# Performance work log

Hardware: AMD Instinct MI355X
Metric: run time of the kernel (lower is better)

Reference implementation:

```python
import jax, jax.numpy as jnp
import numpy as np

V = 50000   # nodes
E = 600000  # edges
D = 256     # node_feat_size == graph_feat_size
K = 20      # hardcoded Kronecker projection dim
OUT = 256   # out_dim

def layer_norm(x, g, b, eps=1e-5):
    mu = jnp.mean(x, axis=-1, keepdims=True)
    var = jnp.var(x, axis=-1, keepdims=True)
    return (x - mu) * jax.lax.rsqrt(var + eps) * g + b

def setup_inputs() -> dict:
    key = jax.random.key(0)
    ks = jax.random.split(key, 12)
    def rn(k, shape, s=0.05):
        return jax.random.normal(k, shape, dtype=jnp.float32) * s
    return dict(
        node_feats=jax.random.normal(ks[0], (V, D), dtype=jnp.float32),
        src=jax.random.randint(ks[1], (E,), 0, V),
        dst=jax.random.randint(ks[2], (E,), 0, V),
        # KroneckerMessage.proj_node: Linear(D,20)+LN(20)
        Wp=rn(ks[3], (D, K)), bp=jnp.zeros((K,), jnp.float32),
        gp=jnp.ones((K,), jnp.float32), betap=jnp.zeros((K,), jnp.float32),
        # KroneckerMessage.proj_kron: Linear(400,OUT)+LN(OUT)
        Wk=rn(ks[4], (K * K, OUT)), bk=jnp.zeros((OUT,), jnp.float32),
        gk=jnp.ones((OUT,), jnp.float32), betak=jnp.zeros((OUT,), jnp.float32),
        # project_edge: Linear(2D,1)
        We=rn(ks[5], (2 * D, 1)), be=jnp.zeros((1,), jnp.float32),
        # AttentiveGRU2.project_node: Linear(D, graph_feat_size=D)
        Wn=rn(ks[6], (D, D)), bn=jnp.zeros((D,), jnp.float32),
        # GRUCell(input=D, hidden=D), torch layout [3H, in]
        W_ih=rn(ks[7], (3 * D, D)), W_hh=rn(ks[8], (3 * D, D)),
        b_ih=jnp.zeros((3 * D,), jnp.float32), b_hh=jnp.zeros((3 * D,), jnp.float32),
        # layer_norm after GRU
        g_ln=jnp.ones((D,), jnp.float32), beta_ln=jnp.zeros((D,), jnp.float32),
        # concat_proj: Linear(D+OUT, D)+LN(D)
        Wc=rn(ks[9], (D + OUT, D)), bc=jnp.zeros((D,), jnp.float32),
        gc=jnp.ones((D,), jnp.float32), betac=jnp.zeros((D,), jnp.float32),
    )

def reference(node_feats, src, dst, Wp, bp, gp, betap, Wk, bk, gk, betak,
              We, be, Wn, bn, W_ih, W_hh, b_ih, b_hh, g_ln, beta_ln,
              Wc, bc, gc, betac):
    Vn = node_feats.shape[0]
    En = src.shape[0]
    # --- KroneckerMessage branch ---
    npj = jax.nn.relu(layer_norm(node_feats @ Wp + bp, gp, betap))        # [V, 20]
    kron = jnp.einsum('ea,ek->eak', npj[src], npj[dst]).reshape(En, -1)    # [E, 400]
    kron = jax.nn.relu(layer_norm(kron @ Wk + bk, gk, betak))              # [E, OUT]
    kron_feat = jax.ops.segment_sum(kron, dst, num_segments=Vn)           # [V, OUT]
    # --- edge attention logits (he = [dst_hv, src_hv]) ---
    he = jnp.concatenate([node_feats[dst], node_feats[src]], axis=1)       # [E, 2D]
    logits = jax.nn.relu(he @ We + be)                                     # [E, 1]
    # --- edge softmax grouped by destination node ---
    m = jax.ops.segment_max(logits, dst, num_segments=Vn)                  # [V, 1]
    ex = jnp.exp(logits - m[dst])
    denom = jax.ops.segment_sum(ex, dst, num_segments=Vn)
    a = ex / denom[dst]                                                    # [E, 1]
    # --- weighted src-feature aggregation ---
    hv = node_feats @ Wn + bn                                              # [V, D]
    context = jax.nn.relu(jax.ops.segment_sum(hv[src] * a, dst, num_segments=Vn))
    # --- GRUCell(context, node_feats), torch semantics ---
    gi = context @ W_ih.T + b_ih
    gh = node_feats @ W_hh.T + b_hh
    i_r, i_z, i_n = jnp.split(gi, 3, axis=1)
    h_r, h_z, h_n = jnp.split(gh, 3, axis=1)
    r = jax.nn.sigmoid(i_r + h_r)
    z = jax.nn.sigmoid(i_z + h_z)
    n = jnp.tanh(i_n + r * h_n)
    h = (1.0 - z) * n + z * node_feats
    gru_out = layer_norm(jax.nn.relu(h), g_ln, beta_ln)                    # [V, D]
    # --- concat + projection ---
    cat = jnp.concatenate([gru_out, kron_feat], axis=1)                    # [V, D+OUT]
    return jax.nn.relu(layer_norm(cat @ Wc + bc, gc, betac))               # [V, D]
```

## Files before the change

kernel.cpp:

```cpp
#include <hip/hip_runtime.h>
#include <hip/hip_bf16.h>
#include <math.h>

#define KG 4
#define KCHUNK 128

typedef __attribute__((ext_vector_type(8))) short bfrag;
typedef __attribute__((ext_vector_type(4))) float cfrag;

__device__ __forceinline__ ushort f2bf(float f) {
    __hip_bfloat16 h = __float2bfloat16(f);
    return *(ushort*)&h;
}
__device__ __forceinline__ float bf2f(ushort u) {
    __hip_bfloat16 h;
    *(ushort*)&h = u;
    return __bfloat162float(h);
}

__device__ __forceinline__ void blockSum2(float& s1, float& s2, float* red) {
    #pragma unroll
    for (int off = 32; off > 0; off >>= 1) {
        s1 += __shfl_xor(s1, off);
        s2 += __shfl_xor(s2, off);
    }
    int lane = threadIdx.x & 63, wid = threadIdx.x >> 6;
    if (lane == 0) { red[wid] = s1; red[4 + wid] = s2; }
    __syncthreads();
    s1 = red[0] + red[1] + red[2] + red[3];
    s2 = red[4] + red[5] + red[6] + red[7];
}

__device__ __forceinline__ float dppWaveSum(float x) {
    float t;
    t = __int_as_float(__builtin_amdgcn_update_dpp(0, __float_as_int(x), 0x111, 0xf, 0xf, true)); x += t;
    t = __int_as_float(__builtin_amdgcn_update_dpp(0, __float_as_int(x), 0x112, 0xf, 0xf, true)); x += t;
    t = __int_as_float(__builtin_amdgcn_update_dpp(0, __float_as_int(x), 0x114, 0xf, 0xf, true)); x += t;
    t = __int_as_float(__builtin_amdgcn_update_dpp(0, __float_as_int(x), 0x118, 0xf, 0xf, true)); x += t;
    t = __int_as_float(__builtin_amdgcn_update_dpp(0, __float_as_int(x), 0x142, 0xf, 0xf, true)); x += t;
    t = __int_as_float(__builtin_amdgcn_update_dpp(0, __float_as_int(x), 0x143, 0xf, 0xf, true)); x += t;
    return __int_as_float(__builtin_amdgcn_readlane(__float_as_int(x), 63));
}

__device__ __forceinline__ float sigmoidf(float x) { return 1.0f / (1.0f + expf(-x)); }

__global__ __launch_bounds__(256) void cast_bf16_kernel(
    const float* __restrict__ x, ushort* __restrict__ y, int n)
{
    int i = (blockIdx.x * 256 + threadIdx.x) * 4;
    if (i < n) {
        float4 v = *(const float4*)(x + i);
        ushort4 o;
        o.x = f2bf(v.x); o.y = f2bf(v.y); o.z = f2bf(v.z); o.w = f2bf(v.w);
        *(ushort4*)(y + i) = o;
    }
}

__global__ __launch_bounds__(256) void prep_w_kernel(
    const float* __restrict__ Wn, const float* __restrict__ Wih,
    const float* __restrict__ Whh, const float* __restrict__ Wc,
    const float* __restrict__ b_ih, const float* __restrict__ b_hh,
    const float* __restrict__ Wp, const float* __restrict__ bp,
    ushort* __restrict__ BTn, ushort* __restrict__ BTrz,
    ushort* __restrict__ BTin, ushort* __restrict__ BThn,
    ushort* __restrict__ BTc, float* __restrict__ bias_rz,
    ushort* __restrict__ BTp, float* __restrict__ bp_pad)
{
    int id = blockIdx.x * 256 + threadIdx.x;
    if (id < 262144) {
        int n = id >> 9, k = id & 511;
        float v = (k < 256) ? Wih[n * 256 + k] : Whh[n * 256 + k - 256];
        BTrz[id] = f2bf(v);
    } else if (id < 327680) {
        int j = id - 262144; int n = j >> 8, k = j & 255;
        BTin[j] = f2bf(Wih[(512 + n) * 256 + k]);
    } else if (id < 393216) {
        int j = id - 327680; int n = j >> 8, k = j & 255;
        BThn[j] = f2bf(Whh[(512 + n) * 256 + k]);
    } else if (id < 458752) {
        int j = id - 393216; int n = j >> 8, k = j & 255;
        BTn[j] = f2bf(Wn[k * 256 + n]);
    } else if (id < 589824) {
        int j = id - 458752; int n = j >> 9, k = j & 511;
        BTc[j] = f2bf(Wc[k * 256 + n]);
    } else if (id < 590336) {
        int n = id - 589824;
        bias_rz[n] = b_ih[n] + b_hh[n];
    } else if (id < 623104) {
        int j = id - 590336; int n = j >> 8, k = j & 255;
        BTp[j] = f2bf((n < 20) ? Wp[k * 20 + n] : 0.f);
    } else if (id < 623232) {
        int n = id - 623104;
        bp_pad[n] = (n < 20) ? bp[n] : 0.f;
    }
}

__global__ __launch_bounds__(256) void mfma_gemm_kernel(
    const ushort* __restrict__ A1, const ushort* __restrict__ A2, int ksplit, int lda,
    const ushort* __restrict__ B, const float* __restrict__ bias,
    void* __restrict__ Cout, int store_bf16,
    int M, int N, int K, int ldc)
{
    __shared__ ushort As[128 * 64];
    __shared__ ushort Bs[128 * 64];
    int t = threadIdx.x;
    int m0 = blockIdx.x * 128, n0 = blockIdx.y * 128;
    int w = t >> 6, lane = t & 63;
    int q = lane >> 4, r = lane & 15;
    int wm = (w & 1) * 64, wn = (w >> 1) * 64;

    cfrag acc[4][4] = {};

    int srow_base = t >> 3;
    int skc = t & 7;

    for (int k0 = 0; k0 < K; k0 += 64) {
        const ushort* Ap; int kb;
        if (k0 < ksplit) { Ap = A1; kb = k0; } else { Ap = A2; kb = k0 - ksplit; }
        int4 av[4], bv[4];
        #pragma unroll
        for (int i = 0; i < 4; ++i) {
            int row = i * 32 + srow_base;
            int grow = m0 + row;
            av[i] = make_int4(0, 0, 0, 0);
            if (grow < M) av[i] = *(const int4*)(Ap + (size_t)grow * lda + kb + skc * 8);
            bv[i] = *(const int4*)(B + (size_t)(n0 + row) * K + k0 + skc * 8);
        }
        __syncthreads();
        #pragma unroll
        for (int i = 0; i < 4; ++i) {
            int row = i * 32 + srow_base;
            int off = row * 64 + ((skc ^ (row & 7)) * 8);
            *(int4*)&As[off] = av[i];
            *(int4*)&Bs[off] = bv[i];
        }
        __syncthreads();
        #pragma unroll
        for (int s = 0; s < 2; ++s) {
            bfrag af[4], bfr[4];
            int kc = s * 4 + q;
            #pragma unroll
            for (int mi = 0; mi < 4; ++mi) {
                int arow = wm + mi * 16 + r;
                af[mi] = *(const bfrag*)&As[arow * 64 + ((kc ^ (arow & 7)) * 8)];
            }
            #pragma unroll
            for (int ni = 0; ni < 4; ++ni) {
                int brow = wn + ni * 16 + r;
                bfr[ni] = *(const bfrag*)&Bs[brow * 64 + ((kc ^ (brow & 7)) * 8)];
            }
            #pragma unroll
            for (int mi = 0; mi < 4; ++mi)
                #pragma unroll
                for (int ni = 0; ni < 4; ++ni)
                    acc[mi][ni] = __builtin_amdgcn_mfma_f32_16x16x32_bf16(
                        af[mi], bfr[ni], acc[mi][ni], 0, 0, 0);
        }
    }

    float bvld[4];
    #pragma unroll
    for (int ni = 0; ni < 4; ++ni) bvld[ni] = bias[n0 + wn + ni * 16 + r];
    #pragma unroll
    for (int mi = 0; mi < 4; ++mi) {
        #pragma unroll
        for (int v = 0; v < 4; ++v) {
            int grow = m0 + wm + mi * 16 + q * 4 + v;
            if (grow >= M) continue;
            #pragma unroll
            for (int ni = 0; ni < 4; ++ni) {
                int gcol = n0 + wn + ni * 16 + r;
                if (gcol >= N) continue;
                float val = acc[mi][ni][v] + bvld[ni];
                if (store_bf16) ((ushort*)Cout)[(size_t)grow * ldc + gcol] = f2bf(val);
                else            ((float*)Cout)[(size_t)grow * ldc + gcol] = val;
            }
        }
    }
}

__global__ __launch_bounds__(256) void ln20_kernel(
    const float* __restrict__ npj32, const float* __restrict__ gp,
    const float* __restrict__ betap, float* __restrict__ npj, int V)
{
    int wid = threadIdx.x >> 6, j = threadIdx.x & 63;
    int v = blockIdx.x * 4 + wid;
    if (v >= V) return;
    float acc = (j < 20) ? npj32[(size_t)v * 32 + j] : 0.f;
    float s1 = acc, s2 = acc * acc;
    #pragma unroll
    for (int off = 32; off > 0; off >>= 1) {
        s1 += __shfl_xor(s1, off);
        s2 += __shfl_xor(s2, off);
    }
    float mu = s1 * (1.0f / 20.0f);
    float var = s2 * (1.0f / 20.0f) - mu * mu;
    if (j < 20) {
        float y = (acc - mu) * rsqrtf(var + 1e-5f) * gp[j] + betap[j];
        npj[(size_t)v * 20 + j] = fmaxf(y, 0.f);
    }
}

__global__ __launch_bounds__(256) void deg_kernel(const int* __restrict__ dst, int* __restrict__ deg, int E) {
    int e = blockIdx.x * 256 + threadIdx.x;
    if (e < E) atomicAdd(&deg[dst[e]], 1);
}

__global__ __launch_bounds__(1024) void scan_kernel(const int* __restrict__ deg, int* __restrict__ row, int V) {
    __shared__ int wsum[16];
    __shared__ int carry_sh;
    int t = threadIdx.x, lane = t & 63, wid = t >> 6;
    if (t == 0) carry_sh = 0;
    __syncthreads();
    for (int base = 0; base < V; base += 1024) {
        int i = base + t;
        int val = (i < V) ? deg[i] : 0;
        #pragma unroll
        for (int s = 1; s < 64; s <<= 1) {
            int n = __shfl_up(val, s);
            if (lane >= s) val += n;
        }
        if (lane == 63) wsum[wid] = val;
        __syncthreads();
        if (wid == 0) {
            int x = (lane < 16) ? wsum[lane] : 0;
            #pragma unroll
            for (int s = 1; s < 16; s <<= 1) {
                int n = __shfl_up(x, s);
                if (lane >= s) x += n;
            }
            if (lane < 16) wsum[lane] = x;
        }
        __syncthreads();
        int wprefix = (wid > 0) ? wsum[wid - 1] : 0;
        int c = carry_sh;
        int incl = c + wprefix + val;
        if (i < V) row[i + 1] = incl;
        __syncthreads();
        if (t == 1023) carry_sh = incl;
    }
    if (t == 0) row[0] = 0;
}

__global__ __launch_bounds__(256) void scatter_kernel(
    const int* __restrict__ dst, const int* __restrict__ row,
    int* __restrict__ cnt, int* __restrict__ eorder, int E)
{
    int e = blockIdx.x * 256 + threadIdx.x;
    if (e < E) {
        int d = dst[e];
        int pos = row[d] + atomicAdd(&cnt[d], 1);
        eorder[pos] = e;
    }
}

__global__ __launch_bounds__(256) void nodeproj_kernel(
    const float* __restrict__ nf, const float* __restrict__ We,
    float* __restrict__ pd, float* __restrict__ ps, int V)
{
    int wid = threadIdx.x >> 6, lane = threadIdx.x & 63;
    int v = blockIdx.x * 4 + wid;
    if (v >= V) return;
    const float* row = nf + (size_t)v * 256;
    int i = lane * 4;
    float4 x  = *(const float4*)(row + i);
    float4 wd = *(const float4*)(We + i);
    float4 wsv = *(const float4*)(We + 256 + i);
    float sd = x.x * wd.x + x.y * wd.y + x.z * wd.z + x.w * wd.w;
    float ss = x.x * wsv.x + x.y * wsv.y + x.z * wsv.z + x.w * wsv.w;
    #pragma unroll
    for (int off = 32; off > 0; off >>= 1) {
        sd += __shfl_xor(sd, off);
        ss += __shfl_xor(ss, off);
    }
    if (lane == 0) { pd[v] = sd; ps[v] = ss; }
}

__global__ __launch_bounds__(256) void edgeprep_kernel(
    const int* __restrict__ eorder, const int* __restrict__ src, const int* __restrict__ dst,
    const float* __restrict__ pd, const float* __restrict__ ps, const float* __restrict__ be,
    float* __restrict__ logitOrd, int* __restrict__ srcOrd, int E)
{
    int p = blockIdx.x * 256 + threadIdx.x;
    if (p < E) {
        int e = eorder[p];
        int s = src[e], d = dst[e];
        srcOrd[p] = s;
        logitOrd[p] = fmaxf(pd[d] + ps[s] + be[0], 0.f);
    }
}

__global__ __launch_bounds__(256) void kron_kernel(
    const float* __restrict__ npj, const int* __restrict__ srcOrd,
    const int* __restrict__ rowPtr,
    const float* __restrict__ Wk, const float* __restrict__ bk,
    const float* __restrict__ gkv, const float* __restrict__ betak,
    ushort* __restrict__ acat, int V)
{
    __shared__ __hip_bfloat16 T[KG * 20 * 256];
    __shared__ float dsh[KG * 20];
    __shared__ float sE[KCHUNK * 20];
    int t = threadIdx.x;
    int v0 = blockIdx.x * KG;

    if (t < KG * 20) {
        int g = t / 20, k = t % 20;
        int v = v0 + g;
        dsh[t] = (v < V) ? npj[(size_t)v * 20 + k] : 0.f;
    }
    __syncthreads();

    float dreg[KG][20];
    #pragma unroll
    for (int g = 0; g < KG; ++g)
        #pragma unroll
        for (int k = 0; k < 20; ++k) dreg[g][k] = dsh[g * 20 + k];

    for (int a = 0; a < 20; ++a) {
        float wv[20];
        #pragma unroll
        for (int k = 0; k < 20; ++k) wv[k] = Wk[(size_t)(a * 20 + k) * 256 + t];
        #pragma unroll
        for (int g = 0; g < KG; ++g) {
            float s = 0.f;
            #pragma unroll
            for (int k = 0; k < 20; ++k) s += dreg[g][k] * wv[k];
            T[(g * 20 + a) * 256 + t] = __float2bfloat16(s);
        }
    }
    __syncthreads();

    int wid = t >> 6, lane = t & 63;
    int v = v0 + wid;
    int c0 = lane * 4;

    float Tr[20][4];
    #pragma unroll
    for (int a = 0; a < 20; ++a) {
        const __hip_bfloat16* tp = &T[(wid * 20 + a) * 256 + c0];
        Tr[a][0] = __bfloat162float(tp[0]);
        Tr[a][1] = __bfloat162float(tp[1]);
        Tr[a][2] = __bfloat162float(tp[2]);
        Tr[a][3] = __bfloat162float(tp[3]);
    }
    float4 bkv = *(const float4*)(bk + c0);
    float4 gk4 = *(const float4*)(gkv + c0);
    float4 bt4 = *(const float4*)(betak + c0);

    int eBase = rowPtr[v0];
    int vEnd = (v0 + KG < V) ? (v0 + KG) : V;
    int eEndB = rowPtr[vEnd];
    int myE0 = (v < V) ? rowPtr[v] : 0;
    int myE1 = (v < V) ? rowPtr[v + 1] : 0;

    float a0 = 0.f, a1 = 0.f, a2 = 0.f, a3 = 0.f;

    for (int base = eBase; base < eEndB; base += KCHUNK) {
        int nC = eEndB - base; if (nC > KCHUNK) nC = KCHUNK;
        __syncthreads();
        for (int idx = t; idx < nC * 20; idx += 256) {
            int le = idx / 20, aa = idx - le * 20;
            sE[idx] = npj[(size_t)srcOrd[base + le] * 20 + aa];
        }
        __syncthreads();

        int lo = (myE0 > base) ? myE0 : base;
        int hi = (myE1 < base + nC) ? myE1 : base + nC;
        int p = lo;
        for (; p + 1 < hi; p += 2) {
            const float* sa = &sE[(p - base) * 20];
            const float* sb = &sE[(p + 1 - base) * 20];
            float4 sa0 = *(const float4*)(sa);
            float4 sa1 = *(const float4*)(sa + 4);
            float4 sa2 = *(const float4*)(sa + 8);
            float4 sa3 = *(const float4*)(sa + 12);
            float4 sa4 = *(const float4*)(sa + 16);
            float4 sb0 = *(const float4*)(sb);
            float4 sb1 = *(const float4*)(sb + 4);
            float4 sb2 = *(const float4*)(sb + 8);
            float4 sb3 = *(const float4*)(sb + 12);
            float4 sb4 = *(const float4*)(sb + 16);
            float sav[20] = {sa0.x, sa0.y, sa0.z, sa0.w, sa1.x, sa1.y, sa1.z, sa1.w,
                             sa2.x, sa2.y, sa2.z, sa2.w, sa3.x, sa3.y, sa3.z, sa3.w,
                             sa4.x, sa4.y, sa4.z, sa4.w};
            float sbv[20] = {sb0.x, sb0.y, sb0.z, sb0.w, sb1.x, sb1.y, sb1.z, sb1.w,
                             sb2.x, sb2.y, sb2.z, sb2.w, sb3.x, sb3.y, sb3.z, sb3.w,
                             sb4.x, sb4.y, sb4.z, sb4.w};
            float ya0 = bkv.x, ya1 = bkv.y, ya2 = bkv.z, ya3 = bkv.w;
            float yb0 = bkv.x, yb1 = bkv.y, yb2 = bkv.z, yb3 = bkv.w;
            #pragma unroll
            for (int a = 0; a < 20; ++a) {
                float va = sav[a], vb = sbv[a];
                ya0 += va * Tr[a][0]; ya1 += va * Tr[a][1];
                ya2 += va * Tr[a][2]; ya3 += va * Tr[a][3];
                yb0 += vb * Tr[a][0]; yb1 += vb * Tr[a][1];
                yb2 += vb * Tr[a][2]; yb3 += vb * Tr[a][3];
            }
            float s1a = dppWaveSum(ya0 + ya1 + ya2 + ya3);
            float s2a = dppWaveSum(ya0 * ya0 + ya1 * ya1 + ya2 * ya2 + ya3 * ya3);
            float s1b = dppWaveSum(yb0 + yb1 + yb2 + yb3);
            float s2b = dppWaveSum(yb0 * yb0 + yb1 * yb1 + yb2 * yb2 + yb3 * yb3);
            float mua = s1a * (1.0f / 256.0f);
            float rsa = rsqrtf(s2a * (1.0f / 256.0f) - mua * mua + 1e-5f);
            float mub = s1b * (1.0f / 256.0f);
            float rsb = rsqrtf(s2b * (1.0f / 256.0f) - mub * mub + 1e-5f);
            a0 += fmaxf((ya0 - mua) * rsa * gk4.x + bt4.x, 0.f) + fmaxf((yb0 - mub) * rsb * gk4.x + bt4.x, 0.f);
            a1 += fmaxf((ya1 - mua) * rsa * gk4.y + bt4.y, 0.f) + fmaxf((yb1 - mub) * rsb * gk4.y + bt4.y, 0.f);
            a2 += fmaxf((ya2 - mua) * rsa * gk4.z + bt4.z, 0.f) + fmaxf((yb2 - mub) * rsb * gk4.z + bt4.z, 0.f);
            a3 += fmaxf((ya3 - mua) * rsa * gk4.w + bt4.w, 0.f) + fmaxf((yb3 - mub) * rsb * gk4.w + bt4.w, 0.f);
        }
        if (p < hi) {
            const float* sa = &sE[(p - base) * 20];
            float4 sa0 = *(const float4*)(sa);
            float4 sa1 = *(const float4*)(sa + 4);
            float4 sa2 = *(const float4*)(sa + 8);
            float4 sa3 = *(const float4*)(sa + 12);
            float4 sa4 = *(const float4*)(sa + 16);
            float sav[20] = {sa0.x, sa0.y, sa0.z, sa0.w, sa1.x, sa1.y, sa1.z, sa1.w,
                             sa2.x, sa2.y, sa2.z, sa2.w, sa3.x, sa3.y, sa3.z, sa3.w,
                             sa4.x, sa4.y, sa4.z, sa4.w};
            float ya0 = bkv.x, ya1 = bkv.y, ya2 = bkv.z, ya3 = bkv.w;
            #pragma unroll
            for (int a = 0; a < 20; ++a) {
                float va = sav[a];
                ya0 += va * Tr[a][0]; ya1 += va * Tr[a][1];
                ya2 += va * Tr[a][2]; ya3 += va * Tr[a][3];
            }
            float s1a = dppWaveSum(ya0 + ya1 + ya2 + ya3);
            float s2a = dppWaveSum(ya0 * ya0 + ya1 * ya1 + ya2 * ya2 + ya3 * ya3);
            float mua = s1a * (1.0f / 256.0f);
            float rsa = rsqrtf(s2a * (1.0f / 256.0f) - mua * mua + 1e-5f);
            a0 += fmaxf((ya0 - mua) * rsa * gk4.x + bt4.x, 0.f);
            a1 += fmaxf((ya1 - mua) * rsa * gk4.y + bt4.y, 0.f);
            a2 += fmaxf((ya2 - mua) * rsa * gk4.z + bt4.z, 0.f);
            a3 += fmaxf((ya3 - mua) * rsa * gk4.w + bt4.w, 0.f);
        }
    }
    if (v < V) {
        ushort4 o;
        o.x = f2bf(a0); o.y = f2bf(a1); o.z = f2bf(a2); o.w = f2bf(a3);
        *(ushort4*)(acat + (size_t)v * 512 + 256 + c0) = o;
    }
}

__global__ __launch_bounds__(256) void att_kernel(
    const float* __restrict__ logitOrd, const int* __restrict__ rowPtr,
    float* __restrict__ mArr, float* __restrict__ invArr, int V)
{
    int wid = threadIdx.x >> 6, lane = threadIdx.x & 63;
    int v = blockIdx.x * 4 + wid;
    if (v >= V) return;
    int e0 = rowPtr[v], e1 = rowPtr[v + 1];
    float m = -1e30f;
    for (int p = e0 + lane; p < e1; p += 64) m = fmaxf(m, logitOrd[p]);
    #pragma unroll
    for (int off = 32; off > 0; off >>= 1) m = fmaxf(m, __shfl_xor(m, off));
    float d = 0.f;
    for (int p = e0 + lane; p < e1; p += 64) d += expf(logitOrd[p] - m);
    #pragma unroll
    for (int off = 32; off > 0; off >>= 1) d += __shfl_xor(d, off);
    if (lane == 0) {
        mArr[v] = m;
        invArr[v] = (e1 > e0) ? (1.0f / d) : 0.f;
    }
}

__global__ __launch_bounds__(256) void ctx_kernel(
    const ushort* __restrict__ hv_bf, const float* __restrict__ logitOrd,
    const float* __restrict__ mArr, const float* __restrict__ invArr,
    const int* __restrict__ srcOrd, const int* __restrict__ rowPtr,
    ushort* __restrict__ ctx_bf, int V)
{
    int v = blockIdx.x;
    int t = threadIdx.x;
    int e0 = rowPtr[v], e1 = rowPtr[v + 1];
    float m = mArr[v], inv = invArr[v];
    float acc = 0.f;
    int p = e0;
    for (; p + 3 < e1; p += 4) {
        int s0 = srcOrd[p], s1 = srcOrd[p + 1], s2 = srcOrd[p + 2], s3 = srcOrd[p + 3];
        float w0 = expf(logitOrd[p] - m) * inv;
        float w1 = expf(logitOrd[p + 1] - m) * inv;
        float w2 = expf(logitOrd[p + 2] - m) * inv;
        float w3 = expf(logitOrd[p + 3] - m) * inv;
        float h0 = bf2f(hv_bf[(size_t)s0 * 256 + t]);
        float h1 = bf2f(hv_bf[(size_t)s1 * 256 + t]);
        float h2 = bf2f(hv_bf[(size_t)s2 * 256 + t]);
        float h3 = bf2f(hv_bf[(size_t)s3 * 256 + t]);
        acc += w0 * h0 + w1 * h1 + w2 * h2 + w3 * h3;
    }
    for (; p < e1; ++p) {
        float wgt = expf(logitOrd[p] - m) * inv;
        acc += wgt * bf2f(hv_bf[(size_t)srcOrd[p] * 256 + t]);
    }
    ctx_bf[(size_t)v * 256 + t] = f2bf(fmaxf(acc, 0.f));
}

__global__ __launch_bounds__(256) void gru_ln_kernel(
    const ushort* __restrict__ rz, const ushort* __restrict__ inb,
    const ushort* __restrict__ hnb, const float* __restrict__ nf,
    const float* __restrict__ g_ln, const float* __restrict__ b_ln,
    ushort* __restrict__ acat, int V)
{
    __shared__ float red[8];
    int v = blockIdx.x, t = threadIdx.x;
    float r = sigmoidf(bf2f(rz[(size_t)v * 512 + t]));
    float z = sigmoidf(bf2f(rz[(size_t)v * 512 + 256 + t]));
    float n = tanhf(bf2f(inb[(size_t)v * 256 + t]) + r * bf2f(hnb[(size_t)v * 256 + t]));
    float h = (1.f - z) * n + z * nf[(size_t)v * 256 + t];
    float x = fmaxf(h, 0.f);
    float s1 = x, s2 = x * x;
    blockSum2(s1, s2, red);
    float mu = s1 * (1.0f / 256.0f);
    float var = s2 * (1.0f / 256.0f) - mu * mu;
    float y = (x - mu) * rsqrtf(var + 1e-5f) * g_ln[t] + b_ln[t];
    acat[(size_t)v * 512 + t] = f2bf(y);
}

__global__ __launch_bounds__(256) void ln_kernel(
    const float* __restrict__ in, float* __restrict__ out,
    const float* __restrict__ g, const float* __restrict__ b, int relu_after)
{
    __shared__ float red[8];
    int v = blockIdx.x, t = threadIdx.x;
    float x = in[(size_t)v * 256 + t];
    float s1 = x, s2 = x * x;
    blockSum2(s1, s2, red);
    float mu = s1 * (1.0f / 256.0f);
    float var = s2 * (1.0f / 256.0f) - mu * mu;
    float y = (x - mu) * rsqrtf(var + 1e-5f) * g[t] + b[t];
    if (relu_after) y = fmaxf(y, 0.f);
    out[(size_t)v * 256 + t] = y;
}

extern "C" void kernel_launch(void* const* d_in, const int* in_sizes, int n_in,
                              void* d_out, int out_size, void* d_ws, size_t ws_size,
                              hipStream_t stream)
{
    const float* nf    = (const float*)d_in[0];
    const int*   src   = (const int*)d_in[1];
    const int*   dst   = (const int*)d_in[2];
    const float* Wp    = (const float*)d_in[3];
    const float* bp    = (const float*)d_in[4];
    const float* gp    = (const float*)d_in[5];
    const float* betap = (const float*)d_in[6];
    const float* Wk    = (const float*)d_in[7];
    const float* bk    = (const float*)d_in[8];
    const float* gk    = (const float*)d_in[9];
    const float* betak = (const float*)d_in[10];
    const float* We    = (const float*)d_in[11];
    const float* be    = (const float*)d_in[12];
    const float* Wn    = (const float*)d_in[13];
    const float* bn    = (const float*)d_in[14];
    const float* W_ih  = (const float*)d_in[15];
    const float* W_hh  = (const float*)d_in[16];
    const float* b_ih  = (const float*)d_in[17];
    const float* b_hh  = (const float*)d_in[18];
    const float* g_ln  = (const float*)d_in[19];
    const float* bt_ln = (const float*)d_in[20];
    const float* Wc    = (const float*)d_in[21];
    const float* bc    = (const float*)d_in[22];
    const float* gc    = (const float*)d_in[23];
    const float* betac = (const float*)d_in[24];

    int V = in_sizes[0] / 256;
    int E = in_sizes[1];

    char* w = (char*)d_ws;
    auto alloc = [&](size_t bytes) -> char* {
        char* p = w;
        w += (bytes + 255) & ~(size_t)255;
        return p;
    };
    float*  npj      = (float*)alloc((size_t)V * 20 * 4);
    float*  npj32    = (float*)alloc((size_t)V * 32 * 4);
    ushort* acat     = (ushort*)alloc((size_t)V * 512 * 2);
    ushort* nf_bf    = (ushort*)alloc((size_t)V * 256 * 2);
    ushort* ctx_bf   = (ushort*)alloc((size_t)V * 256 * 2);
    ushort* rz_bf    = (ushort*)alloc((size_t)V * 512 * 2);
    ushort* hv_bf    = rz_bf;
    ushort* in_bf    = (ushort*)alloc((size_t)V * 256 * 2);
    ushort* hn_bf    = (ushort*)alloc((size_t)V * 256 * 2);
    ushort* BTn      = (ushort*)alloc(65536 * 2);
    ushort* BTrz     = (ushort*)alloc(262144 * 2);
    ushort* BTin     = (ushort*)alloc(65536 * 2);
    ushort* BThn     = (ushort*)alloc(65536 * 2);
    ushort* BTc      = (ushort*)alloc(131072 * 2);
    ushort* BTp      = (ushort*)alloc(32768 * 2);
    float*  bias_rz  = (float*)alloc(512 * 4);
    float*  bp_pad   = (float*)alloc(128 * 4);
    float*  logitOrd = (float*)alloc((size_t)E * 4);
    int*    srcOrd   = (int*)alloc((size_t)E * 4);
    float*  pd       = (float*)alloc((size_t)V * 4);
    float*  ps       = (float*)alloc((size_t)V * 4);
    float*  mArr     = (float*)alloc((size_t)V * 4);
    float*  invArr   = (float*)alloc((size_t)V * 4);
    int*    deg      = (int*)alloc((size_t)V * 4);
    int*    cnt      = (int*)alloc((size_t)V * 4);
    int*    rowp     = (int*)alloc((size_t)(V + 1) * 4);
    int*    eorder   = (int*)alloc((size_t)E * 4);

    hipMemsetAsync(deg, 0, (size_t)V * 4, stream);
    hipMemsetAsync(cnt, 0, (size_t)V * 4, stream);

    int mt = (V + 127) / 128;

    cast_bf16_kernel<<<(V * 64 + 255) / 256, 256, 0, stream>>>(nf, nf_bf, V * 256);
    prep_w_kernel<<<(623232 + 255) / 256, 256, 0, stream>>>(
        Wn, W_ih, W_hh, Wc, b_ih, b_hh, Wp, bp,
        BTn, BTrz, BTin, BThn, BTc, bias_rz, BTp, bp_pad);

    mfma_gemm_kernel<<<dim3(mt, 1), 256, 0, stream>>>(
        nf_bf, nf_bf, 256, 256, BTp, bp_pad, npj32, 0, V, 32, 256, 32);
    ln20_kernel<<<(V + 3) / 4, 256, 0, stream>>>(npj32, gp, betap, npj, V);

    deg_kernel<<<(E + 255) / 256, 256, 0, stream>>>(dst, deg, E);
    scan_kernel<<<1, 1024, 0, stream>>>(deg, rowp, V);
    scatter_kernel<<<(E + 255) / 256, 256, 0, stream>>>(dst, rowp, cnt, eorder, E);
    nodeproj_kernel<<<(V + 3) / 4, 256, 0, stream>>>(nf, We, pd, ps, V);
    edgeprep_kernel<<<(E + 255) / 256, 256, 0, stream>>>(
        eorder, src, dst, pd, ps, be, logitOrd, srcOrd, E);

    mfma_gemm_kernel<<<dim3(mt, 2), 256, 0, stream>>>(
        nf_bf, nf_bf, 256, 256, BTn, bn, hv_bf, 1, V, 256, 256, 256);
    att_kernel<<<(V + 3) / 4, 256, 0, stream>>>(logitOrd, rowp, mArr, invArr, V);
    ctx_kernel<<<V, 256, 0, stream>>>(hv_bf, logitOrd, mArr, invArr, srcOrd, rowp, ctx_bf, V);

    kron_kernel<<<(V + KG - 1) / KG, 256, 0, stream>>>(
        npj, srcOrd, rowp, Wk, bk, gk, betak, acat, V);

    mfma_gemm_kernel<<<dim3(mt, 4), 256, 0, stream>>>(
        ctx_bf, nf_bf, 256, 256, BTrz, bias_rz, rz_bf, 1, V, 512, 512, 512);
    mfma_gemm_kernel<<<dim3(mt, 2), 256, 0, stream>>>(
        ctx_bf, ctx_bf, 256, 256, BTin, b_ih + 512, in_bf, 1, V, 256, 256, 256);
    mfma_gemm_kernel<<<dim3(mt, 2), 256, 0, stream>>>(
        nf_bf, nf_bf, 256, 256, BThn, b_hh + 512, hn_bf, 1, V, 256, 256, 256);

    gru_ln_kernel<<<V, 256, 0, stream>>>(rz_bf, in_bf, hn_bf, nf, g_ln, bt_ln, acat, V);

    mfma_gemm_kernel<<<dim3(mt, 2), 256, 0, stream>>>(
        acat, acat, 512, 512, BTc, bc, (float*)d_out, 0, V, 256, 512, 256);
    ln_kernel<<<V, 256, 0, stream>>>((float*)d_out, (float*)d_out, gc, betac, 1);
}
```

Before: 1.273 ms.

## Precompute per-destination Kronecker tables via chunked MFMA GEMM before edge aggregation

Factors the Kronecker projection so each destination node's 20x256 table T = npj[dst] ⊗ Wk is built with a bf16 MFMA GEMM over node chunks. A new kron2 kernel then only needs a 20-term dot product per edge against register-held table rows, followed by LayerNorm, ReLU and accumulation. This moves the per-block table construction out of the old kron kernel onto matrix cores. In exchange it writes and reads a large bf16 intermediate for each chunk and adds extra launches. It falls back to the old kernel when workspace is too small.

```diff
diff --git a/kernel.cpp b/kernel.cpp
--- a/kernel.cpp
+++ b/kernel.cpp
@@ -4,6 +4,7 @@
 
 #define KG 4
 #define KCHUNK 128
+#define NCHUNKS 8
 
 typedef __attribute__((ext_vector_type(8))) short bfrag;
 typedef __attribute__((ext_vector_type(4))) float cfrag;
@@ -61,10 +62,12 @@
     const float* __restrict__ Whh, const float* __restrict__ Wc,
     const float* __restrict__ b_ih, const float* __restrict__ b_hh,
     const float* __restrict__ Wp, const float* __restrict__ bp,
+    const float* __restrict__ Wk,
     ushort* __restrict__ BTn, ushort* __restrict__ BTrz,
     ushort* __restrict__ BTin, ushort* __restrict__ BThn,
     ushort* __restrict__ BTc, float* __restrict__ bias_rz,
-    ushort* __restrict__ BTp, float* __restrict__ bp_pad)
+    ushort* __restrict__ BTp, float* __restrict__ bp_pad,
+    ushort* __restrict__ W2t)
 {
     int id = blockIdx.x * 256 + threadIdx.x;
     if (id < 262144) {
@@ -92,6 +95,11 @@
     } else if (id < 623232) {
         int n = id - 623104;
         bp_pad[n] = (n < 20) ? bp[n] : 0.f;
+    } else if (id < 950912) {
+        int j = id - 623232;
+        int n = j >> 6, k = j & 63;
+        int a = n >> 8, o = n & 255;
+        W2t[j] = f2bf((k < 20) ? Wk[(size_t)(a * 20 + k) * 256 + o] : 0.f);
     }
 }
 
@@ -181,7 +189,8 @@
 
 __global__ __launch_bounds__(256) void ln20_kernel(
     const float* __restrict__ npj32, const float* __restrict__ gp,
-    const float* __restrict__ betap, float* __restrict__ npj, int V)
+    const float* __restrict__ betap, float* __restrict__ npj,
+    ushort* __restrict__ npj64, int V)
 {
     int wid = threadIdx.x >> 6, j = threadIdx.x & 63;
     int v = blockIdx.x * 4 + wid;
@@ -195,10 +204,13 @@
     }
     float mu = s1 * (1.0f / 20.0f);
     float var = s2 * (1.0f / 20.0f) - mu * mu;
+    float yr = 0.f;
     if (j < 20) {
         float y = (acc - mu) * rsqrtf(var + 1e-5f) * gp[j] + betap[j];
-        npj[(size_t)v * 20 + j] = fmaxf(y, 0.f);
-    }
+        yr = fmaxf(y, 0.f);
+        npj[(size_t)v * 20 + j] = yr;
+    }
+    npj64[(size_t)v * 64 + j] = f2bf(yr);
 }
 
 __global__ __launch_bounds__(256) void deg_kernel(const int* __restrict__ dst, int* __restrict__ deg, int E) {
@@ -287,6 +299,135 @@
         int s = src[e], d = dst[e];
         srcOrd[p] = s;
         logitOrd[p] = fmaxf(pd[d] + ps[s] + be[0], 0.f);
+    }
+}
+
+__global__ __launch_bounds__(256) void kron2_kernel(
+    const float* __restrict__ npj, const int* __restrict__ srcOrd,
+    const int* __restrict__ rowPtr, const ushort* __restrict__ Tb,
+    const float* __restrict__ bk, const float* __restrict__ gkv,
+    const float* __restrict__ betak, ushort* __restrict__ acat,
+    int vlo, int vhi)
+{
+    __shared__ float sE[KCHUNK * 20];
+    int t = threadIdx.x;
+    int v0 = vlo + blockIdx.x * KG;
+    int wid = t >> 6, lane = t & 63;
+    int v = v0 + wid;
+    int c0 = lane * 4;
+
+    float Tr[20][4];
+    if (v < vhi) {
+        const ushort* trow = Tb + (size_t)(v - vlo) * 5120;
+        #pragma unroll
+        for (int a = 0; a < 20; ++a) {
+            ushort4 u = *(const ushort4*)(trow + a * 256 + c0);
+            Tr[a][0] = bf2f(u.x); Tr[a][1] = bf2f(u.y);
+            Tr[a][2] = bf2f(u.z); Tr[a][3] = bf2f(u.w);
+        }
+    } else {
+        #pragma unroll
+        for (int a = 0; a < 20; ++a) {
+            Tr[a][0] = 0.f; Tr[a][1] = 0.f; Tr[a][2] = 0.f; Tr[a][3] = 0.f;
+        }
+    }
+    float4 bkv = *(const float4*)(bk + c0);
+    float4 gk4 = *(const float4*)(gkv + c0);
+    float4 bt4 = *(const float4*)(betak + c0);
+
+    int eBase = rowPtr[v0];
+    int vEnd = (v0 + KG < vhi) ? (v0 + KG) : vhi;
+    int eEndB = rowPtr[vEnd];
+    int myE0 = (v < vhi) ? rowPtr[v] : 0;
+    int myE1 = (v < vhi) ? rowPtr[v + 1] : 0;
+
+    float a0 = 0.f, a1 = 0.f, a2 = 0.f, a3 = 0.f;
+
+    for (int base = eBase; base < eEndB; base += KCHUNK) {
+        int nC = eEndB - base; if (nC > KCHUNK) nC = KCHUNK;
+        __syncthreads();
+        for (int idx = t; idx < nC * 20; idx += 256) {
+            int le = idx / 20, aa = idx - le * 20;
+            sE[idx] = npj[(size_t)srcOrd[base + le] * 20 + aa];
+        }
+        __syncthreads();
+
+        int lo = (myE0 > base) ? myE0 : base;
+        int hi = (myE1 < base + nC) ? myE1 : base + nC;
+        int p = lo;
+        for (; p + 1 < hi; p += 2) {
+            const float* sa = &sE[(p - base) * 20];
+            const float* sb = &sE[(p + 1 - base) * 20];
+            float4 sa0 = *(const float4*)(sa);
+            float4 sa1 = *(const float4*)(sa + 4);
+            float4 sa2 = *(const float4*)(sa + 8);
+            float4 sa3 = *(const float4*)(sa + 12);
+            float4 sa4 = *(const float4*)(sa + 16);
+            float4 sb0 = *(const float4*)(sb);
+            float4 sb1 = *(const float4*)(sb + 4);
+            float4 sb2 = *(const float4*)(sb + 8);
+            float4 sb3 = *(const float4*)(sb + 12);
+            float4 sb4 = *(const float4*)(sb + 16);
+            float sav[20] = {sa0.x, sa0.y, sa0.z, sa0.w, sa1.x, sa1.y, sa1.z, sa1.w,
+                             sa2.x, sa2.y, sa2.z, sa2.w, sa3.x, sa3.y, sa3.z, sa3.w,
+                             sa4.x, sa4.y, sa4.z, sa4.w};
+            float sbv[20] = {sb0.x, sb0.y, sb0.z, sb0.w, sb1.x, sb1.y, sb1.z, sb1.w,
+                             sb2.x, sb2.y, sb2.z, sb2.w, sb3.x, sb3.y, sb3.z, sb3.w,
+                             sb4.x, sb4.y, sb4.z, sb4.w};
+            float ya0 = bkv.x, ya1 = bkv.y, ya2 = bkv.z, ya3 = bkv.w;
+            float yb0 = bkv.x, yb1 = bkv.y, yb2 = bkv.z, yb3 = bkv.w;
+            #pragma unroll
+            for (int a = 0; a < 20; ++a) {
+                float va = sav[a], vb = sbv[a];
+                ya0 += va * Tr[a][0]; ya1 += va * Tr[a][1];
+                ya2 += va * Tr[a][2]; ya3 += va * Tr[a][3];
+                yb0 += vb * Tr[a][0]; yb1 += vb * Tr[a][1];
+                yb2 += vb * Tr[a][2]; yb3 += vb * Tr[a][3];
+            }
+            float s1a = dppWaveSum(ya0 + ya1 + ya2 + ya3);
+            float s2a = dppWaveSum(ya0 * ya0 + ya1 * ya1 + ya2 * ya2 + ya3 * ya3);
+            float s1b = dppWaveSum(yb0 + yb1 + yb2 + yb3);
+            float s2b = dppWaveSum(yb0 * yb0 + yb1 * yb1 + yb2 * yb2 + yb3 * yb3);
+            float mua = s1a * (1.0f / 256.0f);
+            float rsa = rsqrtf(s2a * (1.0f / 256.0f) - mua * mua + 1e-5f);
+            float mub = s1b * (1.0f / 256.0f);
+            float rsb = rsqrtf(s2b * (1.0f / 256.0f) - mub * mub + 1e-5f);
+            a0 += fmaxf((ya0 - mua) * rsa * gk4.x + bt4.x, 0.f) + fmaxf((yb0 - mub) * rsb * gk4.x + bt4.x, 0.f);
+            a1 += fmaxf((ya1 - mua) * rsa * gk4.y + bt4.y, 0.f) + fmaxf((yb1 - mub) * rsb * gk4.y + bt4.y, 0.f);
+            a2 += fmaxf((ya2 - mua) * rsa * gk4.z + bt4.z, 0.f) + fmaxf((yb2 - mub) * rsb * gk4.z + bt4.z, 0.f);
+            a3 += fmaxf((ya3 - mua) * rsa * gk4.w + bt4.w, 0.f) + fmaxf((yb3 - mub) * rsb * gk4.w + bt4.w, 0.f);
+        }
+        if (p < hi) {
+            const float* sa = &sE[(p - base) * 20];
+            float4 sa0 = *(const float4*)(sa);
+            float4 sa1 = *(const float4*)(sa + 4);
+            float4 sa2 = *(const float4*)(sa + 8);
+            float4 sa3 = *(const float4*)(sa + 12);
+            float4 sa4 = *(const float4*)(sa + 16);
+            float sav[20] = {sa0.x, sa0.y, sa0.z, sa0.w, sa1.x, sa1.y, sa1.z, sa1.w,
+                             sa2.x, sa2.y, sa2.z, sa2.w, sa3.x, sa3.y, sa3.z, sa3.w,
+                             sa4.x, sa4.y, sa4.z, sa4.w};
+            float ya0 = bkv.x, ya1 = bkv.y, ya2 = bkv.z, ya3 = bkv.w;
+            #pragma unroll
+            for (int a = 0; a < 20; ++a) {
+                float va = sav[a];
+                ya0 += va * Tr[a][0]; ya1 += va * Tr[a][1];
+                ya2 += va * Tr[a][2]; ya3 += va * Tr[a][3];
+            }
+            float s1a = dppWaveSum(ya0 + ya1 + ya2 + ya3);
+            float s2a = dppWaveSum(ya0 * ya0 + ya1 * ya1 + ya2 * ya2 + ya3 * ya3);
+            float mua = s1a * (1.0f / 256.0f);
+            float rsa = rsqrtf(s2a * (1.0f / 256.0f) - mua * mua + 1e-5f);
+            a0 += fmaxf((ya0 - mua) * rsa * gk4.x + bt4.x, 0.f);
+            a1 += fmaxf((ya1 - mua) * rsa * gk4.y + bt4.y, 0.f);
+            a2 += fmaxf((ya2 - mua) * rsa * gk4.z + bt4.z, 0.f);
+            a3 += fmaxf((ya3 - mua) * rsa * gk4.w + bt4.w, 0.f);
+        }
+    }
+    if (v < vhi) {
+        ushort4 o;
+        o.x = f2bf(a0); o.y = f2bf(a1); o.z = f2bf(a2); o.w = f2bf(a3);
+        *(ushort4*)(acat + (size_t)v * 512 + 256 + c0) = o;
     }
 }
 
@@ -599,20 +740,31 @@
     int*    cnt      = (int*)alloc((size_t)V * 4);
     int*    rowp     = (int*)alloc((size_t)(V + 1) * 4);
     int*    eorder   = (int*)alloc((size_t)E * 4);
+    ushort* npj64    = (ushort*)alloc((size_t)V * 64 * 2);
+    ushort* W2t      = (ushort*)alloc((size_t)5120 * 64 * 2);
+    float*  zbias    = (float*)alloc(5120 * 4);
+
+    int chunkV = (V + NCHUNKS - 1) / NCHUNKS;
+    size_t tbytes = (size_t)chunkV * 5120 * 2;
+    size_t used = (size_t)(w - (char*)d_ws);
+    bool newpath = (used + tbytes + 256) <= ws_size;
+    ushort* T_bf = nullptr;
+    if (newpath) T_bf = (ushort*)alloc(tbytes);
 
     hipMemsetAsync(deg, 0, (size_t)V * 4, stream);
     hipMemsetAsync(cnt, 0, (size_t)V * 4, stream);
+    hipMemsetAsync(zbias, 0, 5120 * 4, stream);
 
     int mt = (V + 127) / 128;
 
     cast_bf16_kernel<<<(V * 64 + 255) / 256, 256, 0, stream>>>(nf, nf_bf, V * 256);
-    prep_w_kernel<<<(623232 + 255) / 256, 256, 0, stream>>>(
-        Wn, W_ih, W_hh, Wc, b_ih, b_hh, Wp, bp,
-        BTn, BTrz, BTin, BThn, BTc, bias_rz, BTp, bp_pad);
+    prep_w_kernel<<<(950912 + 255) / 256, 256, 0, stream>>>(
+        Wn, W_ih, W_hh, Wc, b_ih, b_hh, Wp, bp, Wk,
+        BTn, BTrz, BTin, BThn, BTc, bias_rz, BTp, bp_pad, W2t);
 
     mfma_gemm_kernel<<<dim3(mt, 1), 256, 0, stream>>>(
         nf_bf, nf_bf, 256, 256, BTp, bp_pad, npj32, 0, V, 32, 256, 32);
-    ln20_kernel<<<(V + 3) / 4, 256, 0, stream>>>(npj32, gp, betap, npj, V);
+    ln20_kernel<<<(V + 3) / 4, 256, 0, stream>>>(npj32, gp, betap, npj, npj64, V);
 
     deg_kernel<<<(E + 255) / 256, 256, 0, stream>>>(dst, deg, E);
     scan_kernel<<<1, 1024, 0, stream>>>(deg, rowp, V);
@@ -626,8 +778,22 @@
     att_kernel<<<(V + 3) / 4, 256, 0, stream>>>(logitOrd, rowp, mArr, invArr, V);
     ctx_kernel<<<V, 256, 0, stream>>>(hv_bf, logitOrd, mArr, invArr, srcOrd, rowp, ctx_bf, V);
 
-    kron_kernel<<<(V + KG - 1) / KG, 256, 0, stream>>>(
-        npj, srcOrd, rowp, Wk, bk, gk, betak, acat, V);
+    if (newpath) {
+        for (int c = 0; c < NCHUNKS; ++c) {
+            int vlo = c * chunkV;
+            if (vlo >= V) break;
+            int vhi = vlo + chunkV; if (vhi > V) vhi = V;
+            int cm = vhi - vlo;
+            mfma_gemm_kernel<<<dim3((cm + 127) / 128, 40), 256, 0, stream>>>(
+                npj64 + (size_t)vlo * 64, npj64 + (size_t)vlo * 64, 64, 64,
+                W2t, zbias, T_bf, 1, cm, 5120, 64, 5120);
+            kron2_kernel<<<(cm + KG - 1) / KG, 256, 0, stream>>>(
+                npj, srcOrd, rowp, T_bf, bk, gk, betak, acat, vlo, vhi);
+        }
+    } else {
+        kron_kernel<<<(V + KG - 1) / KG, 256, 0, stream>>>(
+            npj, srcOrd, rowp, Wk, bk, gk, betak, acat, V);
+    }
 
     mfma_gemm_kernel<<<dim3(mt, 4), 256, 0, stream>>>(
         ctx_bf, nf_bf, 256, 256, BTrz, bias_rz, rz_bf, 1, V, 512, 512, 512);
```

Result: no change. 1.276 ms (+0.2%).

## Compute Kronecker intermediate via chunked MFMA GEMM instead of per-block scalar FMAs

Applied to the files above, without the earlier changes.

The per-destination projection T = npj[v] · Wk (reshaped to 20x20x256) used to be computed with scalar FP32 FMAs inside the kron kernel. It is now produced by the existing bf16 MFMA GEMM, using a zero-padded 64-wide npj copy and a pre-transposed Wk. The result is staged in a scratch buffer that reuses in_bf, and the work is split into ten node chunks so each chunk's intermediate is small enough to stay cache-resident before kron2 reads it back. This trades scalar compute and repeated Wk reloads for a large intermediate write and read plus more kernel launches. Each chunk's intermediate (5000×5120 bf16) appears larger than in_bf's original size, so the writes may overrun that buffer.

```diff
diff --git a/kernel.cpp b/kernel.cpp
--- a/kernel.cpp
+++ b/kernel.cpp
@@ -61,10 +61,12 @@
     const float* __restrict__ Whh, const float* __restrict__ Wc,
     const float* __restrict__ b_ih, const float* __restrict__ b_hh,
     const float* __restrict__ Wp, const float* __restrict__ bp,
+    const float* __restrict__ Wk,
     ushort* __restrict__ BTn, ushort* __restrict__ BTrz,
     ushort* __restrict__ BTin, ushort* __restrict__ BThn,
     ushort* __restrict__ BTc, float* __restrict__ bias_rz,
-    ushort* __restrict__ BTp, float* __restrict__ bp_pad)
+    ushort* __restrict__ BTp, float* __restrict__ bp_pad,
+    ushort* __restrict__ W2t)
 {
     int id = blockIdx.x * 256 + threadIdx.x;
     if (id < 262144) {
@@ -92,6 +94,11 @@
     } else if (id < 623232) {
         int n = id - 623104;
         bp_pad[n] = (n < 20) ? bp[n] : 0.f;
+    } else if (id < 950912) {
+        int j = id - 623232;
+        int n = j >> 6, k = j & 63;
+        int a = n >> 8, o = n & 255;
+        W2t[j] = f2bf((k < 20) ? Wk[(size_t)(a * 20 + k) * 256 + o] : 0.f);
     }
 }
 
@@ -181,7 +188,8 @@
 
 __global__ __launch_bounds__(256) void ln20_kernel(
     const float* __restrict__ npj32, const float* __restrict__ gp,
-    const float* __restrict__ betap, float* __restrict__ npj, int V)
+    const float* __restrict__ betap, float* __restrict__ npj,
+    ushort* __restrict__ npj64, int V)
 {
     int wid = threadIdx.x >> 6, j = threadIdx.x & 63;
     int v = blockIdx.x * 4 + wid;
@@ -195,10 +203,13 @@
     }
     float mu = s1 * (1.0f / 20.0f);
     float var = s2 * (1.0f / 20.0f) - mu * mu;
+    float yr = 0.f;
     if (j < 20) {
         float y = (acc - mu) * rsqrtf(var + 1e-5f) * gp[j] + betap[j];
-        npj[(size_t)v * 20 + j] = fmaxf(y, 0.f);
-    }
+        yr = fmaxf(y, 0.f);
+        npj[(size_t)v * 20 + j] = yr;
+    }
+    npj64[(size_t)v * 64 + j] = f2bf(yr);
 }
 
 __global__ __launch_bounds__(256) void deg_kernel(const int* __restrict__ dst, int* __restrict__ deg, int E) {
@@ -290,68 +301,44 @@
     }
 }
 
-__global__ __launch_bounds__(256) void kron_kernel(
+__global__ __launch_bounds__(256) void kron2_kernel(
     const float* __restrict__ npj, const int* __restrict__ srcOrd,
-    const int* __restrict__ rowPtr,
-    const float* __restrict__ Wk, const float* __restrict__ bk,
-    const float* __restrict__ gkv, const float* __restrict__ betak,
-    ushort* __restrict__ acat, int V)
-{
-    __shared__ __hip_bfloat16 T[KG * 20 * 256];
-    __shared__ float dsh[KG * 20];
+    const int* __restrict__ rowPtr, const ushort* __restrict__ Tb,
+    const float* __restrict__ bk, const float* __restrict__ gkv,
+    const float* __restrict__ betak, ushort* __restrict__ acat,
+    int vlo, int vhi)
+{
     __shared__ float sE[KCHUNK * 20];
     int t = threadIdx.x;
-    int v0 = blockIdx.x * KG;
-
-    if (t < KG * 20) {
-        int g = t / 20, k = t % 20;
-        int v = v0 + g;
-        dsh[t] = (v < V) ? npj[(size_t)v * 20 + k] : 0.f;
-    }
-    __syncthreads();
-
-    float dreg[KG][20];
-    #pragma unroll
-    for (int g = 0; g < KG; ++g)
-        #pragma unroll
-        for (int k = 0; k < 20; ++k) dreg[g][k] = dsh[g * 20 + k];
-
-    for (int a = 0; a < 20; ++a) {
-        float wv[20];
-        #pragma unroll
-        for (int k = 0; k < 20; ++k) wv[k] = Wk[(size_t)(a * 20 + k) * 256 + t];
-        #pragma unroll
-        for (int g = 0; g < KG; ++g) {
-            float s = 0.f;
-            #pragma unroll
-            for (int k = 0; k < 20; ++k) s += dreg[g][k] * wv[k];
-            T[(g * 20 + a) * 256 + t] = __float2bfloat16(s);
-        }
-    }
-    __syncthreads();
-
+    int v0 = vlo + blockIdx.x * KG;
     int wid = t >> 6, lane = t & 63;
     int v = v0 + wid;
     int c0 = lane * 4;
 
     float Tr[20][4];
-    #pragma unroll
-    for (int a = 0; a < 20; ++a) {
-        const __hip_bfloat16* tp = &T[(wid * 20 + a) * 256 + c0];
-        Tr[a][0] = __bfloat162float(tp[0]);
-        Tr[a][1] = __bfloat162float(tp[1]);
-        Tr[a][2] = __bfloat162float(tp[2]);
-        Tr[a][3] = __bfloat162float(tp[3]);
+    if (v < vhi) {
+        const ushort* trow = Tb + (size_t)(v - vlo) * 5120;
+        #pragma unroll
+        for (int a = 0; a < 20; ++a) {
+            ushort4 u = *(const ushort4*)(trow + a * 256 + c0);
+            Tr[a][0] = bf2f(u.x); Tr[a][1] = bf2f(u.y);
+            Tr[a][2] = bf2f(u.z); Tr[a][3] = bf2f(u.w);
+        }
+    } else {
+        #pragma unroll
+        for (int a = 0; a < 20; ++a) {
+            Tr[a][0] = 0.f; Tr[a][1] = 0.f; Tr[a][2] = 0.f; Tr[a][3] = 0.f;
+        }
     }
     float4 bkv = *(const float4*)(bk + c0);
     float4 gk4 = *(const float4*)(gkv + c0);
     float4 bt4 = *(const float4*)(betak + c0);
 
     int eBase = rowPtr[v0];
-    int vEnd = (v0 + KG < V) ? (v0 + KG) : V;
+    int vEnd = (v0 + KG < vhi) ? (v0 + KG) : vhi;
     int eEndB = rowPtr[vEnd];
-    int myE0 = (v < V) ? rowPtr[v] : 0;
-    int myE1 = (v < V) ? rowPtr[v + 1] : 0;
+    int myE0 = (v < vhi) ? rowPtr[v] : 0;
+    int myE1 = (v < vhi) ? rowPtr[v + 1] : 0;
 
     float a0 = 0.f, a1 = 0.f, a2 = 0.f, a3 = 0.f;
 
@@ -436,7 +423,7 @@
             a3 += fmaxf((ya3 - mua) * rsa * gk4.w + bt4.w, 0.f);
         }
     }
-    if (v < V) {
+    if (v < vhi) {
         ushort4 o;
         o.x = f2bf(a0); o.y = f2bf(a1); o.z = f2bf(a2); o.w = f2bf(a3);
         *(ushort4*)(acat + (size_t)v * 512 + 256 + c0) = o;
@@ -599,20 +586,27 @@
     int*    cnt      = (int*)alloc((size_t)V * 4);
     int*    rowp     = (int*)alloc((size_t)(V + 1) * 4);
     int*    eorder   = (int*)alloc((size_t)E * 4);
+    ushort* npj64    = (ushort*)alloc((size_t)V * 64 * 2);
+    ushort* W2t      = (ushort*)alloc((size_t)5120 * 64 * 2);
+    float*  zbias    = (float*)alloc(5120 * 4);
+
+    ushort* T_bf = in_bf;
+    int chunkV = V / 10; if (chunkV < 1) chunkV = 1;
 
     hipMemsetAsync(deg, 0, (size_t)V * 4, stream);
     hipMemsetAsync(cnt, 0, (size_t)V * 4, stream);
+    hipMemsetAsync(zbias, 0, 5120 * 4, stream);
 
     int mt = (V + 127) / 128;
 
     cast_bf16_kernel<<<(V * 64 + 255) / 256, 256, 0, stream>>>(nf, nf_bf, V * 256);
-    prep_w_kernel<<<(623232 + 255) / 256, 256, 0, stream>>>(
-        Wn, W_ih, W_hh, Wc, b_ih, b_hh, Wp, bp,
-        BTn, BTrz, BTin, BThn, BTc, bias_rz, BTp, bp_pad);
+    prep_w_kernel<<<(950912 + 255) / 256, 256, 0, stream>>>(
+        Wn, W_ih, W_hh, Wc, b_ih, b_hh, Wp, bp, Wk,
+        BTn, BTrz, BTin, BThn, BTc, bias_rz, BTp, bp_pad, W2t);
 
     mfma_gemm_kernel<<<dim3(mt, 1), 256, 0, stream>>>(
         nf_bf, nf_bf, 256, 256, BTp, bp_pad, npj32, 0, V, 32, 256, 32);
-    ln20_kernel<<<(V + 3) / 4, 256, 0, stream>>>(npj32, gp, betap, npj, V);
+    ln20_kernel<<<(V + 3) / 4, 256, 0, stream>>>(npj32, gp, betap, npj, npj64, V);
 
     deg_kernel<<<(E + 255) / 256, 256, 0, stream>>>(dst, deg, E);
     scan_kernel<<<1, 1024, 0, stream>>>(deg, rowp, V);
@@ -626,8 +620,15 @@
     att_kernel<<<(V + 3) / 4, 256, 0, stream>>>(logitOrd, rowp, mArr, invArr, V);
     ctx_kernel<<<V, 256, 0, stream>>>(hv_bf, logitOrd, mArr, invArr, srcOrd, rowp, ctx_bf, V);
 
-    kron_kernel<<<(V + KG - 1) / KG, 256, 0, stream>>>(
-        npj, srcOrd, rowp, Wk, bk, gk, betak, acat, V);
+    for (int vlo = 0; vlo < V; vlo += chunkV) {
+        int vhi = vlo + chunkV; if (vhi > V) vhi = V;
+        int cm = vhi - vlo;
+        mfma_gemm_kernel<<<dim3((cm + 127) / 128, 40), 256, 0, stream>>>(
+            npj64 + (size_t)vlo * 64, npj64 + (size_t)vlo * 64, 64, 64,
+            W2t, zbias, T_bf, 1, cm, 5120, 64, 5120);
+        kron2_kernel<<<(cm + KG - 1) / KG, 256, 0, stream>>>(
+            npj, srcOrd, rowp, T_bf, bk, gk, betak, acat, vlo, vhi);
+    }
 
     mfma_gemm_kernel<<<dim3(mt, 4), 256, 0, stream>>>(
         ctx_bf, nf_bf, 256, 256, BTrz, bias_rz, rz_bf, 1, V, 512, 512, 512);
```

Measured after the change: 1.456 ms. 1.14x slower.

## Use packed fp16 dot products and 8-node 512-thread blocks in kron kernel

Applied to the files above, without the earlier changes.

Wk is pre-packed once into fp16 pairs, and the per-node T = npj·Wk precompute in the kron kernel now uses fdot2 on packed halves instead of scalar fp32 FMAs. Blocks grow to 8 nodes and 512 threads, so each Wk load is reused across twice as many nodes and the T build is split across two thread halves. This cuts ALU work and global weight traffic per node. The cost is lower precision in T, doubled LDS use for T, and register pressure at 512 threads.

```diff
diff --git a/kernel.cpp b/kernel.cpp
--- a/kernel.cpp
+++ b/kernel.cpp
@@ -2,11 +2,13 @@
 #include <hip/hip_bf16.h>
 #include <math.h>
 
-#define KG 4
+#define KG 8
+#define KTHR 512
 #define KCHUNK 128
 
 typedef __attribute__((ext_vector_type(8))) short bfrag;
 typedef __attribute__((ext_vector_type(4))) float cfrag;
+typedef _Float16 __attribute__((ext_vector_type(2))) half2v;
 
 __device__ __forceinline__ ushort f2bf(float f) {
     __hip_bfloat16 h = __float2bfloat16(f);
@@ -16,6 +18,11 @@
     __hip_bfloat16 h;
     *(ushort*)&h = u;
     return __bfloat162float(h);
+}
+__device__ __forceinline__ uint packf16(float lo, float hi) {
+    _Float16 l = (_Float16)lo, h = (_Float16)hi;
+    ushort ul = *(ushort*)&l, uh = *(ushort*)&h;
+    return (uint)ul | ((uint)uh << 16);
 }
 
 __device__ __forceinline__ void blockSum2(float& s1, float& s2, float* red) {
@@ -61,10 +68,12 @@
     const float* __restrict__ Whh, const float* __restrict__ Wc,
     const float* __restrict__ b_ih, const float* __restrict__ b_hh,
     const float* __restrict__ Wp, const float* __restrict__ bp,
+    const float* __restrict__ Wk,
     ushort* __restrict__ BTn, ushort* __restrict__ BTrz,
     ushort* __restrict__ BTin, ushort* __restrict__ BThn,
     ushort* __restrict__ BTc, float* __restrict__ bias_rz,
-    ushort* __restrict__ BTp, float* __restrict__ bp_pad)
+    ushort* __restrict__ BTp, float* __restrict__ bp_pad,
+    uint* __restrict__ Wkp)
 {
     int id = blockIdx.x * 256 + threadIdx.x;
     if (id < 262144) {
@@ -92,6 +101,13 @@
     } else if (id < 623232) {
         int n = id - 623104;
         bp_pad[n] = (n < 20) ? bp[n] : 0.f;
+    } else if (id < 674432) {
+        int j = id - 623232;
+        int row = j >> 8, o = j & 255;
+        int a = row / 10, kk = row - a * 10;
+        float lo = Wk[(size_t)(a * 20 + 2 * kk) * 256 + o];
+        float hi = Wk[(size_t)(a * 20 + 2 * kk + 1) * 256 + o];
+        Wkp[j] = packf16(lo, hi);
     }
 }
 
@@ -290,42 +306,56 @@
     }
 }
 
-__global__ __launch_bounds__(256) void kron_kernel(
+__global__ __launch_bounds__(KTHR) void kron_kernel(
     const float* __restrict__ npj, const int* __restrict__ srcOrd,
     const int* __restrict__ rowPtr,
-    const float* __restrict__ Wk, const float* __restrict__ bk,
+    const uint* __restrict__ Wkp, const float* __restrict__ bk,
     const float* __restrict__ gkv, const float* __restrict__ betak,
     ushort* __restrict__ acat, int V)
 {
     __shared__ __hip_bfloat16 T[KG * 20 * 256];
-    __shared__ float dsh[KG * 20];
+    __shared__ uint dshp[KG * 10];
     __shared__ float sE[KCHUNK * 20];
     int t = threadIdx.x;
     int v0 = blockIdx.x * KG;
 
-    if (t < KG * 20) {
-        int g = t / 20, k = t % 20;
+    if (t < KG * 10) {
+        int g = t / 10, kk = t - g * 10;
         int v = v0 + g;
-        dsh[t] = (v < V) ? npj[(size_t)v * 20 + k] : 0.f;
+        float lo = 0.f, hi = 0.f;
+        if (v < V) {
+            lo = npj[(size_t)v * 20 + 2 * kk];
+            hi = npj[(size_t)v * 20 + 2 * kk + 1];
+        }
+        dshp[t] = packf16(lo, hi);
     }
     __syncthreads();
 
-    float dreg[KG][20];
-    #pragma unroll
-    for (int g = 0; g < KG; ++g)
+    {
+        uint dreg[KG][10];
         #pragma unroll
-        for (int k = 0; k < 20; ++k) dreg[g][k] = dsh[g * 20 + k];
-
-    for (int a = 0; a < 20; ++a) {
-        float wv[20];
-        #pragma unroll
-        for (int k = 0; k < 20; ++k) wv[k] = Wk[(size_t)(a * 20 + k) * 256 + t];
-        #pragma unroll
-        for (int g = 0; g < KG; ++g) {
-            float s = 0.f;
-            #pragma unroll
-            for (int k = 0; k < 20; ++k) s += dreg[g][k] * wv[k];
-            T[(g * 20 + a) * 256 + t] = __float2bfloat16(s);
+        for (int g = 0; g < KG; ++g)
+            #pragma unroll
+            for (int kk = 0; kk < 10; ++kk) dreg[g][kk] = dshp[g * 10 + kk];
+
+        int c = t & 255, h = t >> 8;
+        int a0 = h * 10;
+        for (int a = a0; a < a0 + 10; ++a) {
+            uint wv[10];
+            #pragma unroll
+            for (int kk = 0; kk < 10; ++kk)
+                wv[kk] = Wkp[(size_t)(a * 10 + kk) * 256 + c];
+            #pragma unroll
+            for (int g = 0; g < KG; ++g) {
+                float s = 0.f;
+                #pragma unroll
+                for (int kk = 0; kk < 10; ++kk) {
+                    half2v d2 = *(half2v*)&dreg[g][kk];
+                    half2v w2 = *(half2v*)&wv[kk];
+                    s = __builtin_amdgcn_fdot2(d2, w2, s, false);
+                }
+                T[(g * 20 + a) * 256 + c] = __float2bfloat16(s);
+            }
         }
     }
     __syncthreads();
@@ -358,7 +388,7 @@
     for (int base = eBase; base < eEndB; base += KCHUNK) {
         int nC = eEndB - base; if (nC > KCHUNK) nC = KCHUNK;
         __syncthreads();
-        for (int idx = t; idx < nC * 20; idx += 256) {
+        for (int idx = t; idx < nC * 20; idx += KTHR) {
             int le = idx / 20, aa = idx - le * 20;
             sE[idx] = npj[(size_t)srcOrd[base + le] * 20 + aa];
         }
@@ -599,6 +629,7 @@
     int*    cnt      = (int*)alloc((size_t)V * 4);
     int*    rowp     = (int*)alloc((size_t)(V + 1) * 4);
     int*    eorder   = (int*)alloc((size_t)E * 4);
+    uint*   Wkp      = (uint*)alloc((size_t)51200 * 4);
 
     hipMemsetAsync(deg, 0, (size_t)V * 4, stream);
     hipMemsetAsync(cnt, 0, (size_t)V * 4, stream);
@@ -606,9 +637,9 @@
     int mt = (V + 127) / 128;
 
     cast_bf16_kernel<<<(V * 64 + 255) / 256, 256, 0, stream>>>(nf, nf_bf, V * 256);
-    prep_w_kernel<<<(623232 + 255) / 256, 256, 0, stream>>>(
-        Wn, W_ih, W_hh, Wc, b_ih, b_hh, Wp, bp,
-        BTn, BTrz, BTin, BThn, BTc, bias_rz, BTp, bp_pad);
+    prep_w_kernel<<<(674432 + 255) / 256, 256, 0, stream>>>(
+        Wn, W_ih, W_hh, Wc, b_ih, b_hh, Wp, bp, Wk,
+        BTn, BTrz, BTin, BThn, BTc, bias_rz, BTp, bp_pad, Wkp);
 
     mfma_gemm_kernel<<<dim3(mt, 1), 256, 0, stream>>>(
         nf_bf, nf_bf, 256, 256, BTp, bp_pad, npj32, 0, V, 32, 256, 32);
@@ -626,8 +657,8 @@
     att_kernel<<<(V + 3) / 4, 256, 0, stream>>>(logitOrd, rowp, mArr, invArr, V);
     ctx_kernel<<<V, 256, 0, stream>>>(hv_bf, logitOrd, mArr, invArr, srcOrd, rowp, ctx_bf, V);
 
-    kron_kernel<<<(V + KG - 1) / KG, 256, 0, stream>>>(
-        npj, srcOrd, rowp, Wk, bk, gk, betak, acat, V);
+    kron_kernel<<<(V + KG - 1) / KG, KTHR, 0, stream>>>(
+        npj, srcOrd, rowp, Wkp, bk, gk, betak, acat, V);
 
     mfma_gemm_kernel<<<dim3(mt, 4), 256, 0, stream>>>(
         ctx_bf, nf_bf, 256, 256, BTrz, bias_rz, rz_bf, 1, V, 512, 512, 512);
```

Result: faster. 1.227 ms (-3.6%).
